# Optimization experiments

Hardware: AMD Instinct MI355X
Metric: run time of the kernel (lower is better)

The kernel has to match this reference:

```python
import jax, jax.numpy as jnp
import numpy as np

CHUNK = 1024  # rows of pc0 processed per tile to avoid materializing the full NxM matrix


def _min_sqdist(a, b):
    """For each row of a [N,3], min squared distance to rows of b [M,3]."""
    b_sq = jnp.sum(b * b, axis=1)  # [M]

    def tile_min(ac):  # ac: [CHUNK, 3]
        d = jnp.sum(ac * ac, axis=1)[:, None] + b_sq[None, :] - 2.0 * (ac @ b.T)
        return jnp.min(d, axis=1)

    n, dim = a.shape
    return jax.lax.map(tile_min, a.reshape(n // CHUNK, CHUNK, dim)).reshape(n)


def setup_inputs() -> dict:
    key = jax.random.key(0)
    k0, k1 = jax.random.split(key)
    pc0 = jax.random.normal(k0, (65536, 3), dtype=jnp.float32)
    pc1 = jax.random.normal(k1, (65536, 3), dtype=jnp.float32)
    return {"pc0": pc0, "pc1": pc1}


def reference(pc0, pc1):
    # chamfer forward: dist0[i] = min_j ||pc0[i]-pc1[j]||^2
    dist0 = _min_sqdist(pc0, pc1)
    mask = dist0 <= 2.0
    # mean over selected elements (boolean mask is constant wrt grads, as in torch)
    return jnp.sum(jnp.where(mask, dist0, 0.0)) / jnp.sum(mask).astype(dist0.dtype)
```

## Files before the change

kernel.cpp:

```cpp
#include <hip/hip_runtime.h>


constexpr int   NPTS  = 65536;
constexpr int   G     = 64;
constexpr int   NC    = G * G * G;
constexpr float H     = 0.125f;
constexpr float ORG   = -4.0f;
constexpr float INVH  = 8.0f;
constexpr int   G3    = 32;
constexpr float H3    = 0.25f;
constexpr float INVH3 = 4.0f;
constexpr int   BLOCK = 256;
constexpr int   PBLOCKS = 1024;
constexpr int   SB    = 128;
constexpr int   CHUNK = NC / SB;

__device__ __forceinline__ int cellOf(float x) {
  int c = (int)floorf((x - ORG) * INVH);
  return min(max(c, 0), G - 1);
}
__device__ __forceinline__ int cellOf3(float x) {
  int c = (int)floorf((x - ORG) * INVH3);
  return min(max(c, 0), G3 - 1);
}

__global__ __launch_bounds__(BLOCK) void count_kernel(
    const float* __restrict__ pc0, const float* __restrict__ pc1,
    unsigned* __restrict__ counts0, unsigned* __restrict__ counts1) {
  const int gid = blockIdx.x * BLOCK + threadIdx.x;
  const float* p; unsigned* cnt; int i;
  if (gid < NPTS) { p = pc1; cnt = counts1; i = gid; }
  else            { p = pc0; cnt = counts0; i = gid - NPTS; }
  const float x = p[3 * i], y = p[3 * i + 1], z = p[3 * i + 2];
  atomicAdd(&cnt[(cellOf(z) * G + cellOf(y)) * G + cellOf(x)], 1u);
}

__global__ __launch_bounds__(1024) void scan_partial_kernel(
    const unsigned* __restrict__ counts0, const unsigned* __restrict__ counts1,
    unsigned* __restrict__ partials) {
  const unsigned* counts = blockIdx.y ? counts0 : counts1;
  const int base = blockIdx.x * CHUNK + threadIdx.x * 2;
  unsigned sum = counts[base] + counts[base + 1];
  for (int o = 32; o; o >>= 1) sum += __shfl_down(sum, o, 64);
  __shared__ unsigned ws[16];
  if ((threadIdx.x & 63) == 0) ws[threadIdx.x >> 6] = sum;
  __syncthreads();
  if (threadIdx.x == 0) {
    unsigned t = 0;
    for (int w = 0; w < 16; ++w) t += ws[w];
    partials[blockIdx.y * SB + blockIdx.x] = t;
  }
}

__global__ __launch_bounds__(256) void scan_mid_kernel(
    unsigned* __restrict__ partials) {
  const int tid = threadIdx.x;
  const int g   = tid >> 7;
  const int li  = tid & 127;
  const unsigned v = partials[g * SB + li];
  unsigned inc = v;
  for (int o = 1; o < 64; o <<= 1) {
    const unsigned t = __shfl_up(inc, o, 64);
    if ((tid & 63) >= o) inc += t;
  }
  __shared__ unsigned wt[4];
  if ((tid & 63) == 63) wt[tid >> 6] = inc;
  __syncthreads();
  const unsigned woff = ((tid >> 6) & 1) ? wt[g << 1] : 0u;
  partials[g * SB + li] = woff + inc - v;
}

__global__ __launch_bounds__(1024) void scan_final_kernel(
    const unsigned* __restrict__ counts0, unsigned* __restrict__ cur0,
    const unsigned* __restrict__ counts1, unsigned* __restrict__ cur1,
    const unsigned* __restrict__ partials) {
  const unsigned* counts = blockIdx.y ? counts0 : counts1;
  unsigned* cur          = blockIdx.y ? cur0    : cur1;
  const int tid = threadIdx.x;
  const int base = blockIdx.x * CHUNK + tid * 2;
  const unsigned a = counts[base], b = counts[base + 1];
  const unsigned tsum = a + b;
  unsigned inc = tsum;
  for (int o = 1; o < 64; o <<= 1) {
    const unsigned t = __shfl_up(inc, o, 64);
    if ((tid & 63) >= o) inc += t;
  }
  __shared__ unsigned wt[16];
  if ((tid & 63) == 63) wt[tid >> 6] = inc;
  __syncthreads();
  if (tid < 16) {
    unsigned w = wt[tid];
    for (int o = 1; o < 16; o <<= 1) {
      const unsigned t = __shfl_up(w, o, 16);
      if (tid >= o) w += t;
    }
    wt[tid] = w;
  }
  __syncthreads();
  const unsigned woff = (tid >> 6) ? wt[(tid >> 6) - 1] : 0u;
  const unsigned off =
      partials[blockIdx.y * SB + blockIdx.x] + woff + inc - tsum;
  cur[base] = off;
  cur[base + 1] = off + a;
}

__global__ __launch_bounds__(BLOCK) void scatter_kernel(
    const float* __restrict__ pc0, const float* __restrict__ pc1,
    unsigned* __restrict__ cur0, unsigned* __restrict__ cur1,
    float4* __restrict__ q, float4* __restrict__ s) {
  const int gid = blockIdx.x * BLOCK + threadIdx.x;
  const float* p; unsigned* cur; float4* dst; int i;
  if (gid < NPTS) { p = pc1; cur = cur1; dst = s; i = gid; }
  else            { p = pc0; cur = cur0; dst = q; i = gid - NPTS; }
  const float x = p[3 * i], y = p[3 * i + 1], z = p[3 * i + 2];
  const int cid = (cellOf(z) * G + cellOf(y)) * G + cellOf(x);
  dst[atomicAdd(&cur[cid], 1u)] = make_float4(x, y, z, 0.f);
}

__global__ __launch_bounds__(BLOCK) void query_kernel(
    const float4* __restrict__ q, const unsigned* __restrict__ ends,
    const float4* __restrict__ s,
    unsigned* __restrict__ wl, float* __restrict__ wlBest,
    unsigned* __restrict__ pendCnt, float* __restrict__ bkt) {
  const int gtid = blockIdx.x * BLOCK + threadIdx.x;
  const int i   = gtid >> 2;
  const int sub = gtid & 3;
  const float4 p = q[i];
  const int cx = cellOf(p.x), cy = cellOf(p.y), cz = cellOf(p.z);
  const int x0 = max(cx - 1, 0), x1 = min(cx + 1, G - 1);

  unsigned rs[9], re[9];
#pragma unroll
  for (int rr = 0; rr < 9; ++rr) {
    const int zz = cz + rr / 3 - 1, yy = cy + rr % 3 - 1;
    const bool ok = (zz >= 0) && (zz < G) && (yy >= 0) && (yy < G);
    const int rb = ok ? (zz * G + yy) * G : 0;
    rs[rr] = ok ? ((rb + x0) ? ends[rb + x0 - 1] : 0u) : 0u;
    re[rr] = ok ? ends[rb + x1] : 0u;
  }
  float best = 3.4e38f;
#pragma unroll
  for (int rr = 0; rr < 9; ++rr) {
#pragma unroll 4
    for (unsigned j = rs[rr] + sub; j < re[rr]; j += 4) {
      const float4 c = s[j];
      const float dx = p.x - c.x, dy = p.y - c.y, dz = p.z - c.z;
      best = fminf(best, fmaf(dx, dx, fmaf(dy, dy, dz * dz)));
    }
  }
  best = fminf(best, __shfl_xor(best, 1, 64));
  best = fminf(best, __shfl_xor(best, 2, 64));

  float v = 0.f, c = 0.f;
  if (sub == 0) {
    if (best > H * H) {
      const unsigned k = atomicAdd(pendCnt, 1u);
      wl[k] = (unsigned)i; wlBest[k] = best;
    } else if (best <= 2.0f) { v = best; c = 1.0f; }
  }

  for (int o = 32; o; o >>= 1) {
    v += __shfl_down(v, o, 64);
    c += __shfl_down(c, o, 64);
  }
  __shared__ float wsum[BLOCK / 64], wcnt[BLOCK / 64];
  const int wid = threadIdx.x >> 6;
  if ((threadIdx.x & 63) == 0) { wsum[wid] = v; wcnt[wid] = c; }
  __syncthreads();
  if (threadIdx.x == 0) {
    float bv = 0.f, bc = 0.f;
    for (int w = 0; w < BLOCK / 64; ++w) { bv += wsum[w]; bc += wcnt[w]; }
    if (bc != 0.f) {
      atomicAdd(&bkt[2 * (blockIdx.x & 63) + 0], bv);
      atomicAdd(&bkt[2 * (blockIdx.x & 63) + 1], bc);
    }
  }
}

__global__ __launch_bounds__(BLOCK) void pending_kernel(
    const float4* __restrict__ q,
    const unsigned* __restrict__ ends, const float4* __restrict__ s,
    const unsigned* __restrict__ wl, const float* __restrict__ wlBest,
    unsigned* __restrict__ pendCnt, float* __restrict__ bkt,
    unsigned* __restrict__ done, float* __restrict__ out) {
  __shared__ int snP;
  __shared__ float wsum[BLOCK / 64], wcnt[BLOCK / 64];
  __shared__ int isLast;
  __shared__ float fs[BLOCK / 64], fc[BLOCK / 64];
  if (threadIdx.x == 0) snP = (int)atomicAdd(pendCnt, 0u);
  __syncthreads();
  const int lane = threadIdx.x & 63, wid = threadIdx.x >> 6;
  const int gw = blockIdx.x * (BLOCK / 64) + wid;
  const int nW = PBLOCKS * (BLOCK / 64);
  float v = 0.f, c = 0.f;

  for (int it = gw; it < snP; it += nW) {
    const unsigned qi = wl[it];
    const float4 p = q[qi];
    const int cx = cellOf3(p.x), cy = cellOf3(p.y), cz = cellOf3(p.z);
    float best = wlBest[it];

    for (int r = 1; r <= 8; ++r) {
      const float cov = H3 * (float)(r - 1);
      if (best <= cov * cov) break;
      if (best > 2.0f && cov * cov >= 2.0f) break;
      const int S = (r == 1) ? 9 : 8 * r + 2 * (2 * r - 1) * (2 * r - 1);
      float b = best;
      for (int sI = lane; sI < S; sI += 64) {
        int dz, dy, xa, xb;
        if (r == 1) {
          dz = sI / 3 - 1; dy = sI % 3 - 1; xa = cx - 1; xb = cx + 1;
        } else if (sI < 8 * r) {
          if (sI < 2 * r + 1)      { dz = -r; dy = sI - r; }
          else if (sI < 4 * r + 2) { dz =  r; dy = sI - (2 * r + 1) - r; }
          else { const int t2 = sI - (4 * r + 2); dz = (t2 >> 1) - (r - 1);
                 dy = (t2 & 1) ? r : -r; }
          xa = cx - r; xb = cx + r;
        } else {
          const int t2 = sI - 8 * r, ci = t2 >> 1, w1 = 2 * r - 1;
          dz = ci / w1 - (r - 1); dy = ci % w1 - (r - 1);
          xa = xb = (t2 & 1) ? cx + r : cx - r;
        }
        const int Z = cz + dz, Y = cy + dy;
        if (Z < 0 || Z >= G3 || Y < 0 || Y >= G3) continue;
        int a3 = max(xa, 0), e3 = min(xb, G3 - 1);
        if (a3 > e3) continue;
        const float ylo = ORG + (float)Y * H3;
        const float zlo = ORG + (float)Z * H3;
        const float dyd = fmaxf(fmaxf(ylo - p.y, p.y - (ylo + H3)), 0.f);
        const float dzd = fmaxf(fmaxf(zlo - p.z, p.z - (zlo + H3)), 0.f);
        const float dyz2 = dyd * dyd + dzd * dzd;
        const float bnd = fminf(b, 2.0f);
        if (dyz2 >= bnd) continue;
        const float halfx = sqrtf(bnd - dyz2);
        const int xlo = (int)floorf((p.x - halfx - ORG) * INVH3);
        const int xhi = (int)floorf((p.x + halfx - ORG) * INVH3);
        a3 = max(a3, xlo); e3 = min(e3, xhi);
        if (a3 > e3) continue;
        const int xs = 2 * a3, xe = 2 * e3 + 1;
        unsigned js[4], je[4];
#pragma unroll
        for (int k = 0; k < 4; ++k) {
          const int zz = 2 * Z + (k >> 1), yy = 2 * Y + (k & 1);
          const int rb = (zz * G + yy) * G;
          js[k] = (rb + xs) ? ends[rb + xs - 1] : 0u;
          je[k] = ends[rb + xe];
        }
#pragma unroll
        for (int k = 0; k < 4; ++k) {
#pragma unroll 4
          for (unsigned j = js[k]; j < je[k]; ++j) {
            const float4 cd = s[j];
            const float dx = p.x - cd.x, dyv = p.y - cd.y, dzv = p.z - cd.z;
            b = fminf(b, fmaf(dx, dx, fmaf(dyv, dyv, dzv * dzv)));
          }
        }
      }
      for (int o = 32; o; o >>= 1) b = fminf(b, __shfl_xor(b, o, 64));
      best = b;
    }
    if (lane == 0 && best <= 2.0f) { v += best; c += 1.0f; }
  }

  if (lane == 0) { wsum[wid] = v; wcnt[wid] = c; }
  __syncthreads();
  if (threadIdx.x == 0) {
    float bv = 0.f, bc = 0.f;
    for (int w = 0; w < BLOCK / 64; ++w) { bv += wsum[w]; bc += wcnt[w]; }
    if (bc != 0.f) {
      atomicAdd(&bkt[2 * (blockIdx.x & 63) + 0], bv);
      atomicAdd(&bkt[2 * (blockIdx.x & 63) + 1], bc);
    }
    __threadfence();
    isLast = (atomicAdd(done, 1u) == (unsigned)(PBLOCKS - 1));
  }
  __syncthreads();
  if (isLast) {
    const float val = (threadIdx.x < 128) ? atomicAdd(&bkt[threadIdx.x], 0.0f) : 0.0f;
    float sv = (threadIdx.x & 1) ? 0.f : val;
    float cv = (threadIdx.x & 1) ? val : 0.f;
    for (int o = 32; o; o >>= 1) {
      sv += __shfl_down(sv, o, 64);
      cv += __shfl_down(cv, o, 64);
    }
    if (lane == 0) { fs[wid] = sv; fc[wid] = cv; }
    __syncthreads();
    if (threadIdx.x == 0) {
      float S = 0.f, C = 0.f;
      for (int w = 0; w < BLOCK / 64; ++w) { S += fs[w]; C += fc[w]; }
      out[0] = S / C;
    }
  }
}

extern "C" void kernel_launch(void* const* d_in, const int* in_sizes, int n_in,
                              void* d_out, int out_size, void* d_ws, size_t ws_size,
                              hipStream_t stream) {
  const float* pc0 = (const float*)d_in[0];
  const float* pc1 = (const float*)d_in[1];
  float* out = (float*)d_out;

  char* w = (char*)d_ws;
  auto nxt = [&](size_t bytes) {
    char* p = w; w += (bytes + 255) & ~(size_t)255; return p;
  };
  unsigned* counts1  = (unsigned*)nxt((size_t)NC * 4);
  unsigned* counts0  = (unsigned*)nxt((size_t)NC * 4);
  char*     misc     = nxt(1024);
  float*    bkt      = (float*)misc;
  unsigned* done     = (unsigned*)(misc + 512);
  unsigned* pendCnt  = (unsigned*)(misc + 516);
  unsigned* partials = (unsigned*)nxt((size_t)2 * SB * 4);
  unsigned* cur1     = (unsigned*)nxt((size_t)NC * 4);
  unsigned* cur0     = (unsigned*)nxt((size_t)NC * 4);
  float4*   s        = (float4*)nxt((size_t)NPTS * 16);
  float4*   q        = (float4*)nxt((size_t)NPTS * 16);
  unsigned* wl       = (unsigned*)nxt((size_t)NPTS * 4);
  float*    wlBest   = (float*)nxt((size_t)NPTS * 4);

  hipMemsetAsync(counts1, 0, (size_t)2 * NC * 4 + 1024, stream);

  count_kernel<<<2 * NPTS / BLOCK, BLOCK, 0, stream>>>(pc0, pc1, counts0, counts1);
  scan_partial_kernel<<<dim3(SB, 2), 1024, 0, stream>>>(counts0, counts1, partials);
  scan_mid_kernel<<<1, 256, 0, stream>>>(partials);
  scan_final_kernel<<<dim3(SB, 2), 1024, 0, stream>>>(counts0, cur0,
                                                      counts1, cur1, partials);
  scatter_kernel<<<2 * NPTS / BLOCK, BLOCK, 0, stream>>>(
      pc0, pc1, cur0, cur1, q, s);
  query_kernel<<<4 * NPTS / BLOCK, BLOCK, 0, stream>>>(q, cur1, s, wl, wlBest,
                                                       pendCnt, bkt);
  pending_kernel<<<PBLOCKS, BLOCK, 0, stream>>>(q, cur1, s, wl, wlBest,
                                                pendCnt, bkt, done, out);
}
```

Baseline: 139.1 us.

## Fuse the whole chamfer pipeline into one cooperative kernel with grid syncs

Replaces the memset plus seven separate kernel launches (count, three scan stages, scatter, query, pending) with a single cooperative kernel. It uses 256 blocks of 1024 threads, separates the phases with grid-wide barriers, and merges the two count and cursor arrays into one combined scan. The aim is to remove per-launch overhead and inter-kernel gaps, at the price of about nine grid syncs and a fixed one-block-per-CU occupancy for every phase. The old multi-kernel path is kept as a fallback if the cooperative launch fails.

```diff
diff --git a/kernel.cpp b/kernel.cpp
--- a/kernel.cpp
+++ b/kernel.cpp
@@ -1,5 +1,8 @@
 #include <hip/hip_runtime.h>
-
+#include <hip/hip_cooperative_groups.h>
+
+
+namespace cg = cooperative_groups;
 
 constexpr int   NPTS  = 65536;
 constexpr int   G     = 64;
@@ -10,6 +13,11 @@
 constexpr int   G3    = 32;
 constexpr float H3    = 0.25f;
 constexpr float INVH3 = 4.0f;
+
+constexpr int   BLOCK_M = 1024;
+constexpr int   GRID_M  = 256;
+constexpr int   NW_M    = GRID_M * (BLOCK_M / 64);
+
 constexpr int   BLOCK = 256;
 constexpr int   PBLOCKS = 1024;
 constexpr int   SB    = 128;
@@ -22,6 +30,250 @@
 __device__ __forceinline__ int cellOf3(float x) {
   int c = (int)floorf((x - ORG) * INVH3);
   return min(max(c, 0), G3 - 1);
+}
+
+__global__ __launch_bounds__(BLOCK_M, 4) void mega_kernel(
+    const float* __restrict__ pc0, const float* __restrict__ pc1,
+    unsigned* __restrict__ countsAll,
+    unsigned* __restrict__ curAll,
+    unsigned* __restrict__ partials,
+    float4*  __restrict__ sAll,
+    unsigned* __restrict__ wl, float* __restrict__ wlBest,
+    unsigned* __restrict__ pendCnt, float* __restrict__ bkt,
+    float* __restrict__ out)
+{
+  cg::grid_group grid = cg::this_grid();
+  const int tid  = threadIdx.x;
+  const int bid  = blockIdx.x;
+  const int gid  = bid * BLOCK_M + tid;
+  const int lane = tid & 63, wid = tid >> 6;
+
+  __shared__ unsigned shu[16];
+  __shared__ float    shf[32];
+
+  countsAll[2 * gid]     = 0u;
+  countsAll[2 * gid + 1] = 0u;
+  if (bid == 0) {
+    if (tid < 128) bkt[tid] = 0.f;
+    else if (tid == 128) pendCnt[0] = 0u;
+  }
+  grid.sync();
+
+  if (gid < 2 * NPTS) {
+    const float* p; unsigned* cnt; int i;
+    if (gid < NPTS) { p = pc1; cnt = countsAll;      i = gid; }
+    else            { p = pc0; cnt = countsAll + NC; i = gid - NPTS; }
+    const float x = p[3 * i], y = p[3 * i + 1], z = p[3 * i + 2];
+    atomicAdd(&cnt[(cellOf(z) * G + cellOf(y)) * G + cellOf(x)], 1u);
+  }
+  grid.sync();
+
+  {
+    const int base = bid * 2048 + tid * 2;
+    unsigned sum = countsAll[base] + countsAll[base + 1];
+    for (int o = 32; o; o >>= 1) sum += __shfl_down(sum, o, 64);
+    if (lane == 0) shu[wid] = sum;
+    __syncthreads();
+    if (tid == 0) {
+      unsigned t = 0;
+      for (int w = 0; w < 16; ++w) t += shu[w];
+      partials[bid] = t;
+    }
+  }
+  grid.sync();
+
+  if (bid == 0) {
+    const unsigned vv = (tid < 256) ? partials[tid] : 0u;
+    unsigned inc = vv;
+    for (int o = 1; o < 64; o <<= 1) {
+      const unsigned t = __shfl_up(inc, o, 64);
+      if (lane >= o) inc += t;
+    }
+    if (lane == 63 && wid < 4) shu[wid] = inc;
+    __syncthreads();
+    if (tid < 256) {
+      unsigned woff = 0;
+      for (int w = 0; w < wid; ++w) woff += shu[w];
+      partials[tid] = woff + inc - vv;
+    }
+  }
+  grid.sync();
+
+  {
+    const int base = bid * 2048 + tid * 2;
+    const unsigned a = countsAll[base], b2 = countsAll[base + 1];
+    const unsigned ts = a + b2;
+    unsigned inc = ts;
+    for (int o = 1; o < 64; o <<= 1) {
+      const unsigned t = __shfl_up(inc, o, 64);
+      if (lane >= o) inc += t;
+    }
+    if (lane == 63) shu[wid] = inc;
+    __syncthreads();
+    unsigned woff = 0;
+    for (int w = 0; w < wid; ++w) woff += shu[w];
+    const unsigned off = partials[bid] + woff + inc - ts;
+    curAll[base]     = off;
+    curAll[base + 1] = off + a;
+  }
+  grid.sync();
+
+  if (gid < 2 * NPTS) {
+    const float* p; unsigned* cur; int i;
+    if (gid < NPTS) { p = pc1; cur = curAll;      i = gid; }
+    else            { p = pc0; cur = curAll + NC; i = gid - NPTS; }
+    const float x = p[3 * i], y = p[3 * i + 1], z = p[3 * i + 2];
+    const int cid = (cellOf(z) * G + cellOf(y)) * G + cellOf(x);
+    sAll[atomicAdd(&cur[cid], 1u)] = make_float4(x, y, z, 0.f);
+  }
+  grid.sync();
+
+  float accV = 0.f, accC = 0.f;
+
+  {
+    const unsigned* __restrict__ ends = curAll;
+    const int i   = gid >> 2;
+    const int sub = gid & 3;
+    const float4 p = sAll[NPTS + i];
+    const int cx = cellOf(p.x), cy = cellOf(p.y), cz = cellOf(p.z);
+    const int x0 = max(cx - 1, 0), x1 = min(cx + 1, G - 1);
+
+    unsigned rs[9], re[9];
+#pragma unroll
+    for (int rr = 0; rr < 9; ++rr) {
+      const int zz = cz + rr / 3 - 1, yy = cy + rr % 3 - 1;
+      const bool ok = (zz >= 0) && (zz < G) && (yy >= 0) && (yy < G);
+      const int rb = ok ? (zz * G + yy) * G : 0;
+      rs[rr] = ok ? ((rb + x0) ? ends[rb + x0 - 1] : 0u) : 0u;
+      re[rr] = ok ? ends[rb + x1] : 0u;
+    }
+    float best = 3.4e38f;
+#pragma unroll
+    for (int rr = 0; rr < 9; ++rr) {
+#pragma unroll 4
+      for (unsigned j = rs[rr] + sub; j < re[rr]; j += 4) {
+        const float4 cq = sAll[j];
+        const float dx = p.x - cq.x, dy = p.y - cq.y, dz = p.z - cq.z;
+        best = fminf(best, fmaf(dx, dx, fmaf(dy, dy, dz * dz)));
+      }
+    }
+    best = fminf(best, __shfl_xor(best, 1, 64));
+    best = fminf(best, __shfl_xor(best, 2, 64));
+
+    if (sub == 0) {
+      if (best > H * H) {
+        const unsigned k = atomicAdd(pendCnt, 1u);
+        wl[k] = (unsigned)i; wlBest[k] = best;
+      } else if (best <= 2.0f) { accV = best; accC = 1.0f; }
+    }
+  }
+  grid.sync();
+
+  {
+    const unsigned* __restrict__ ends = curAll;
+    const int snP = (int)pendCnt[0];
+    const int gw  = bid * (BLOCK_M / 64) + wid;
+
+    for (int it = gw; it < snP; it += NW_M) {
+      const unsigned qi = wl[it];
+      const float4 p = sAll[NPTS + qi];
+      const int cx = cellOf3(p.x), cy = cellOf3(p.y), cz = cellOf3(p.z);
+      float best = wlBest[it];
+
+      for (int r = 1; r <= 8; ++r) {
+        const float cov = H3 * (float)(r - 1);
+        if (best <= cov * cov) break;
+        if (best > 2.0f && cov * cov >= 2.0f) break;
+        const int S = (r == 1) ? 9 : 8 * r + 2 * (2 * r - 1) * (2 * r - 1);
+        float b = best;
+        for (int sI = lane; sI < S; sI += 64) {
+          int dz, dy, xa, xb;
+          if (r == 1) {
+            dz = sI / 3 - 1; dy = sI % 3 - 1; xa = cx - 1; xb = cx + 1;
+          } else if (sI < 8 * r) {
+            if (sI < 2 * r + 1)      { dz = -r; dy = sI - r; }
+            else if (sI < 4 * r + 2) { dz =  r; dy = sI - (2 * r + 1) - r; }
+            else { const int t2 = sI - (4 * r + 2); dz = (t2 >> 1) - (r - 1);
+                   dy = (t2 & 1) ? r : -r; }
+            xa = cx - r; xb = cx + r;
+          } else {
+            const int t2 = sI - 8 * r, ci = t2 >> 1, w1 = 2 * r - 1;
+            dz = ci / w1 - (r - 1); dy = ci % w1 - (r - 1);
+            xa = xb = (t2 & 1) ? cx + r : cx - r;
+          }
+          const int Z = cz + dz, Y = cy + dy;
+          if (Z < 0 || Z >= G3 || Y < 0 || Y >= G3) continue;
+          int a3 = max(xa, 0), e3 = min(xb, G3 - 1);
+          if (a3 > e3) continue;
+          const float ylo = ORG + (float)Y * H3;
+          const float zlo = ORG + (float)Z * H3;
+          const float dyd = fmaxf(fmaxf(ylo - p.y, p.y - (ylo + H3)), 0.f);
+          const float dzd = fmaxf(fmaxf(zlo - p.z, p.z - (zlo + H3)), 0.f);
+          const float dyz2 = dyd * dyd + dzd * dzd;
+          const float bnd = fminf(b, 2.0f);
+          if (dyz2 >= bnd) continue;
+          const float halfx = sqrtf(bnd - dyz2);
+          const int xlo = (int)floorf((p.x - halfx - ORG) * INVH3);
+          const int xhi = (int)floorf((p.x + halfx - ORG) * INVH3);
+          a3 = max(a3, xlo); e3 = min(e3, xhi);
+          if (a3 > e3) continue;
+          const int xs = 2 * a3, xe = 2 * e3 + 1;
+          unsigned js[4], je[4];
+#pragma unroll
+          for (int k = 0; k < 4; ++k) {
+            const int zz = 2 * Z + (k >> 1), yy = 2 * Y + (k & 1);
+            const int rb = (zz * G + yy) * G;
+            js[k] = (rb + xs) ? ends[rb + xs - 1] : 0u;
+            je[k] = ends[rb + xe];
+          }
+#pragma unroll
+          for (int k = 0; k < 4; ++k) {
+#pragma unroll 4
+            for (unsigned j = js[k]; j < je[k]; ++j) {
+              const float4 cd = sAll[j];
+              const float dx = p.x - cd.x, dyv = p.y - cd.y, dzv = p.z - cd.z;
+              b = fminf(b, fmaf(dx, dx, fmaf(dyv, dyv, dzv * dzv)));
+            }
+          }
+        }
+        for (int o = 32; o; o >>= 1) b = fminf(b, __shfl_xor(b, o, 64));
+        best = b;
+      }
+      if (lane == 0 && best <= 2.0f) { accV += best; accC += 1.0f; }
+    }
+  }
+
+  for (int o = 32; o; o >>= 1) {
+    accV += __shfl_down(accV, o, 64);
+    accC += __shfl_down(accC, o, 64);
+  }
+  if (lane == 0) { shf[wid] = accV; shf[16 + wid] = accC; }
+  __syncthreads();
+  if (tid == 0) {
+    float bv = 0.f, bc = 0.f;
+    for (int w = 0; w < 16; ++w) { bv += shf[w]; bc += shf[16 + w]; }
+    if (bc != 0.f) {
+      atomicAdd(&bkt[2 * (bid & 63) + 0], bv);
+      atomicAdd(&bkt[2 * (bid & 63) + 1], bc);
+    }
+  }
+  grid.sync();
+  if (bid == 0) {
+    const float val = (tid < 128) ? bkt[tid] : 0.f;
+    float sv = (tid & 1) ? 0.f : val;
+    float cv = (tid & 1) ? val : 0.f;
+    for (int o = 32; o; o >>= 1) {
+      sv += __shfl_down(sv, o, 64);
+      cv += __shfl_down(cv, o, 64);
+    }
+    if (lane == 0) { shf[wid] = sv; shf[16 + wid] = cv; }
+    __syncthreads();
+    if (tid == 0) {
+      float S = 0.f, C = 0.f;
+      for (int w = 0; w < 16; ++w) { S += shf[w]; C += shf[16 + w]; }
+      out[0] = S / C;
+    }
+  }
 }
 
 __global__ __launch_bounds__(BLOCK) void count_kernel(
@@ -318,17 +570,26 @@
   unsigned* wl       = (unsigned*)nxt((size_t)NPTS * 4);
   float*    wlBest   = (float*)nxt((size_t)NPTS * 4);
 
-  hipMemsetAsync(counts1, 0, (size_t)2 * NC * 4 + 1024, stream);
-
-  count_kernel<<<2 * NPTS / BLOCK, BLOCK, 0, stream>>>(pc0, pc1, counts0, counts1);
-  scan_partial_kernel<<<dim3(SB, 2), 1024, 0, stream>>>(counts0, counts1, partials);
-  scan_mid_kernel<<<1, 256, 0, stream>>>(partials);
-  scan_final_kernel<<<dim3(SB, 2), 1024, 0, stream>>>(counts0, cur0,
-                                                      counts1, cur1, partials);
-  scatter_kernel<<<2 * NPTS / BLOCK, BLOCK, 0, stream>>>(
-      pc0, pc1, cur0, cur1, q, s);
-  query_kernel<<<4 * NPTS / BLOCK, BLOCK, 0, stream>>>(q, cur1, s, wl, wlBest,
-                                                       pendCnt, bkt);
-  pending_kernel<<<PBLOCKS, BLOCK, 0, stream>>>(q, cur1, s, wl, wlBest,
-                                                pendCnt, bkt, done, out);
-}
+  unsigned* countsAll = counts1;
+  unsigned* curAll    = cur1;
+  float4*   sAll      = s;
+
+  void* args[] = { &pc0, &pc1, &countsAll, &curAll, &partials, &sAll,
+                   &wl, &wlBest, &pendCnt, &bkt, &out };
+  hipError_t ce = hipLaunchCooperativeKernel((void*)mega_kernel, dim3(GRID_M),
+                                             dim3(BLOCK_M), args, 0, stream);
+  if (ce != hipSuccess) {
+    hipMemsetAsync(counts1, 0, (size_t)2 * NC * 4 + 1024, stream);
+    count_kernel<<<2 * NPTS / BLOCK, BLOCK, 0, stream>>>(pc0, pc1, counts0, counts1);
+    scan_partial_kernel<<<dim3(SB, 2), 1024, 0, stream>>>(counts0, counts1, partials);
+    scan_mid_kernel<<<1, 256, 0, stream>>>(partials);
+    scan_final_kernel<<<dim3(SB, 2), 1024, 0, stream>>>(counts0, cur0,
+                                                        counts1, cur1, partials);
+    scatter_kernel<<<2 * NPTS / BLOCK, BLOCK, 0, stream>>>(
+        pc0, pc1, cur0, cur1, q, s);
+    query_kernel<<<4 * NPTS / BLOCK, BLOCK, 0, stream>>>(q, cur1, s, wl, wlBest,
+                                                         pendCnt, bkt);
+    pending_kernel<<<PBLOCKS, BLOCK, 0, stream>>>(q, cur1, s, wl, wlBest,
+                                                  pendCnt, bkt, done, out);
+  }
+}
```

Result: slower. 329.3 us (+136.8%).
